# Kernel tuning notes

Hardware: AMD Instinct MI355X
Metric: run time of the kernel (lower is better)

The kernel has to match this reference:

```python
import jax, jax.numpy as jnp
import numpy as np

N_NODES = 50000
N_EDGES = 800000
N_GRAPHS = 128
IN_DIM = 256
OUT_DIM = 128
N_LAYERS = 3
NEG_SLOPE = 0.01  # nn.LeakyReLU default


def setup_inputs() -> dict:
    key = jax.random.key(0)
    ks = jax.random.split(key, 10)
    feat = jax.random.normal(ks[0], (N_NODES, IN_DIM), jnp.float32)
    src = jax.random.randint(ks[1], (N_EDGES,), 0, N_NODES, jnp.int32)
    dst = jax.random.randint(ks[2], (N_EDGES,), 0, N_NODES, jnp.int32)
    graph_ids = jnp.sort(jax.random.randint(ks[3], (N_NODES,), 0, N_GRAPHS, jnp.int32))
    s_in = 1.0 / np.sqrt(IN_DIM).astype(np.float32)
    s_out = 1.0 / np.sqrt(OUT_DIM).astype(np.float32)
    w_red = jax.random.uniform(ks[4], (IN_DIM, OUT_DIM), jnp.float32, -s_in, s_in)
    b_red = jax.random.uniform(ks[5], (OUT_DIM,), jnp.float32, -s_in, s_in)
    w_gcn = jax.random.uniform(ks[6], (N_LAYERS, OUT_DIM, OUT_DIM), jnp.float32, -s_out, s_out)
    b_gcn = jnp.zeros((N_LAYERS, OUT_DIM), jnp.float32)  # DGL GraphConv bias init = zeros
    w_cls = jax.random.uniform(ks[7], (OUT_DIM, 2), jnp.float32, -s_out, s_out)
    b_cls = jax.random.uniform(ks[8], (2,), jnp.float32, -s_out, s_out)
    return dict(feat=feat, src=src, dst=dst, graph_ids=graph_ids,
                w_red=w_red, b_red=b_red, w_gcn=w_gcn, b_gcn=b_gcn,
                w_cls=w_cls, b_cls=b_cls)


def _graph_conv(x, src, dst, w, b, out_norm, in_norm):
    # DGL GraphConv, norm='both': h = D_in^{-1/2} A D_out^{-1/2} x W + b
    xs = x * out_norm[:, None]                                   # [N, d] source normalization
    agg = jax.ops.segment_sum(xs[src], dst, num_segments=x.shape[0])  # gather -> scatter-add
    return (agg * in_norm[:, None]) @ w + b


def reference(feat, src, dst, graph_ids, w_red, b_red, w_gcn, b_gcn, w_cls, b_cls):
    n = feat.shape[0]
    ones = jnp.ones((src.shape[0],), feat.dtype)
    out_deg = jax.ops.segment_sum(ones, src, num_segments=n)
    in_deg = jax.ops.segment_sum(ones, dst, num_segments=n)
    out_norm = jnp.maximum(out_deg, 1.0) ** -0.5  # DGL clamps degree to >=1
    in_norm = jnp.maximum(in_deg, 1.0) ** -0.5
    h0 = feat @ w_red + b_red  # Dropout(0.2) in eval mode = identity
    # Faithful to source: every layer consumes h0 (node_features never updated);
    # only the last layer's activation survives the loop.
    out = h0
    for i in range(N_LAYERS):
        out = jax.nn.leaky_relu(
            _graph_conv(h0, src, dst, w_gcn[i], b_gcn[i], out_norm, in_norm), NEG_SLOPE)
    g = jax.ops.segment_sum(out, graph_ids, num_segments=N_GRAPHS)  # sum readout per graph
    return g @ w_cls + b_cls  # [N_GRAPHS, 2]
```

## Files before the change

### kernel.cpp

```cpp
#include <hip/hip_runtime.h>

#define N_NODES 50000
#define N_EDGES 800000
#define N_GRAPHS 128
#define IN_DIM 256
#define OUT_DIM 128
#define NEG_SLOPE 0.01f

#define RCHUNK 64
#define NB_SCAN ((N_NODES + 255) / 256)

#define NSLICE 4
#define SLICE 12544
#define NTOT (NSLICE * SLICE)
#define NCHUNK 64
#define NE4 (N_EDGES / 4)
#define QPC (NE4 / NCHUNK)

typedef __attribute__((ext_vector_type(8))) short bf16x8;
typedef __attribute__((ext_vector_type(4))) float f32x4;
typedef unsigned short ushort_t;
typedef unsigned int uint_t;

__device__ inline ushort_t f2b(float f) {
    union { float f; unsigned u; } c{f};
    unsigned r = c.u + 0x7FFFu + ((c.u >> 16) & 1u);
    return (ushort_t)(r >> 16);
}
__device__ inline float b2f(ushort_t u) {
    union { unsigned u; float f; } c{(unsigned)u << 16};
    return c.f;
}
__device__ inline float blo(uint_t v) {
    union { unsigned u; float f; } c{v << 16};
    return c.f;
}
__device__ inline float bhi(uint_t v) {
    union { unsigned u; float f; } c{v & 0xFFFF0000u};
    return c.f;
}

__global__ __launch_bounds__(256) void deg_kernel(const int4* __restrict__ src4,
                                                  const int4* __restrict__ dst4,
                                                  ushort_t* __restrict__ rep) {
    __shared__ uint_t bins[SLICE / 2];
    int b     = blockIdx.x;
    int hist  = b >> 8;
    int rem   = b & 255;
    int slice = rem >> 6;
    int chunk = rem & 63;
    const int4* ea = hist ? dst4 : src4;
    int lo = slice * SLICE;

    for (int i = threadIdx.x; i < SLICE / 2; i += 256) bins[i] = 0;
    __syncthreads();

    int q0 = chunk * QPC;
    int q1 = q0 + QPC;
    for (int q = q0 + threadIdx.x; q < q1; q += 256) {
        int4 e = ea[q];
        unsigned a0 = (unsigned)(e.x - lo);
        if (a0 < SLICE) atomicAdd(&bins[a0 >> 1], 1u << ((a0 & 1) << 4));
        unsigned a1 = (unsigned)(e.y - lo);
        if (a1 < SLICE) atomicAdd(&bins[a1 >> 1], 1u << ((a1 & 1) << 4));
        unsigned a2 = (unsigned)(e.z - lo);
        if (a2 < SLICE) atomicAdd(&bins[a2 >> 1], 1u << ((a2 & 1) << 4));
        unsigned a3 = (unsigned)(e.w - lo);
        if (a3 < SLICE) atomicAdd(&bins[a3 >> 1], 1u << ((a3 & 1) << 4));
    }
    __syncthreads();

    uint_t* rp32 = (uint_t*)(rep + (size_t)(hist * NCHUNK + chunk) * NTOT + lo);
    for (int i = threadIdx.x; i < SLICE / 2; i += 256)
        rp32[i] = bins[i];
}

__global__ __launch_bounds__(256) void norm_kernel(ushort_t* __restrict__ rep,
                                                   float* __restrict__ out_norm,
                                                   float* __restrict__ in_norm,
                                                   int* __restrict__ deg_in_tot,
                                                   int* __restrict__ bsum) {
    __shared__ int red[256];
    int t = threadIdx.x;
    int i = blockIdx.x * 256 + t;
    int si_keep = 0;
    if (i < N_NODES) {
        int so = 0;
#pragma unroll
        for (int c = 0; c < NCHUNK; ++c) so += rep[(size_t)c * NTOT + i];
        int si = 0;
#pragma unroll
        for (int c = 0; c < NCHUNK; ++c) {
            size_t off = (size_t)(NCHUNK + c) * NTOT + i;
            int v = rep[off];
            rep[off] = (ushort_t)si;
            si += v;
        }
        deg_in_tot[i] = si;
        si_keep = si;
        int dq = so > 1 ? so : 1;
        int di = si > 1 ? si : 1;
        out_norm[i] = rsqrtf((float)dq);
        in_norm[i]  = rsqrtf((float)di);
    }
    red[t] = si_keep;
    __syncthreads();
    for (int off = 128; off > 0; off >>= 1) {
        if (t < off) red[t] += red[t + off];
        __syncthreads();
    }
    if (t == 0) bsum[blockIdx.x] = red[0];
}

__global__ __launch_bounds__(256) void fillwc_kernel(const int* __restrict__ deg_in,
                                                     const int* __restrict__ bsum,
                                                     int* __restrict__ row_ofs,
                                                     const float* __restrict__ w_red,
                                                     const float* __restrict__ b_red,
                                                     const float* __restrict__ w2,
                                                     ushort_t* __restrict__ Wcs,
                                                     float* __restrict__ bc,
                                                     float* __restrict__ g) {
    int t   = threadIdx.x;
    int bid = blockIdx.x;

    if (bid < NB_SCAN) {
        __shared__ int sh[256];
        int v = (t < NB_SCAN) ? bsum[t] : 0;
        sh[t] = v;
        __syncthreads();
        for (int off = 1; off < 256; off <<= 1) {
            int a = sh[t];
            int b = (t >= off) ? sh[t - off] : 0;
            __syncthreads();
            sh[t] = a + b;
            __syncthreads();
        }
        int bofs  = sh[bid] - bsum[bid];
        int total = sh[NB_SCAN - 1];
        __syncthreads();

        int idx = bid * 256 + t;
        int dv  = (idx < N_NODES) ? deg_in[idx] : 0;
        sh[t] = dv;
        __syncthreads();
        for (int off = 1; off < 256; off <<= 1) {
            int a = sh[t];
            int b = (t >= off) ? sh[t - off] : 0;
            __syncthreads();
            sh[t] = a + b;
            __syncthreads();
        }
        if (idx < N_NODES) row_ofs[idx] = bofs + sh[t] - dv;
        if (bid == 0 && t == 0) row_ofs[N_NODES] = total;
    } else if (t < OUT_DIM) {
        int i = bid - NB_SCAN;
        int j = t;
        if (i < N_GRAPHS) g[i * OUT_DIM + j] = 0.f;
        const float* vin = (i < IN_DIM) ? (w_red + (size_t)i * OUT_DIM) : b_red;
        float s = 0.f;
        for (int k = 0; k < OUT_DIM; ++k) s = fmaf(vin[k], w2[k * OUT_DIM + j], s);
        if (i < IN_DIM) Wcs[(size_t)j * IN_DIM + i] = f2b(s);
        else            bc[j] = s;
    }
}

__global__ __launch_bounds__(256) void build_kernel(const int4* __restrict__ src4,
                                                    const int4* __restrict__ dst4,
                                                    const int* __restrict__ row_ofs,
                                                    const ushort_t* __restrict__ rep,
                                                    int* __restrict__ esrc) {
    __shared__ int cur[SLICE];
    int b     = blockIdx.x;
    int slice = b >> 6;
    int chunk = b & 63;
    int lo    = slice * SLICE;
    const ushort_t* rel = rep + (size_t)(NCHUNK + chunk) * NTOT + lo;

    for (int i = threadIdx.x; i < SLICE; i += 256) {
        int n = lo + i;
        int r = (n < N_NODES) ? row_ofs[n] : 0;
        cur[i] = r + (int)rel[i];
    }
    __syncthreads();

    int q0 = chunk * QPC;
    int q1 = q0 + QPC;
    for (int q = q0 + threadIdx.x; q < q1; q += 256) {
        int4 s = src4[q];
        int4 d = dst4[q];
        unsigned a0 = (unsigned)(d.x - lo); if (a0 < SLICE) esrc[atomicAdd(&cur[a0], 1)] = s.x;
        unsigned a1 = (unsigned)(d.y - lo); if (a1 < SLICE) esrc[atomicAdd(&cur[a1], 1)] = s.y;
        unsigned a2 = (unsigned)(d.z - lo); if (a2 < SLICE) esrc[atomicAdd(&cur[a2], 1)] = s.z;
        unsigned a3 = (unsigned)(d.w - lo); if (a3 < SLICE) esrc[atomicAdd(&cur[a3], 1)] = s.w;
    }
}

__global__ __launch_bounds__(256) void gemm_z(const float* __restrict__ feat,
                                              const ushort_t* __restrict__ Wcs,
                                              const float* __restrict__ bc,
                                              const float* __restrict__ out_norm,
                                              ushort_t* __restrict__ zb) {
    __shared__ ushort_t Bs[64 * IN_DIM];
    int t    = threadIdx.x;
    int lane = t & 63;
    int wv   = t >> 6;
    int bm   = blockIdx.x * 64 + wv * 16;
    int bn0  = blockIdx.y * 64;
    int mrow = lane & 15;
    int kg   = lane >> 4;
    int gm   = bm + mrow;

    {
        const char* wsrc = (const char*)(Wcs + (size_t)bn0 * IN_DIM);
        char* bdst = (char*)Bs;
#pragma unroll
        for (int p = 0; p < 8; ++p) {
            int d  = p * 4096 + t * 16;
            int ds = d ^ (((d >> 9) & 7) << 4);
            *(int4*)(bdst + ds) = *(const int4*)(wsrc + d);
        }
    }
    __syncthreads();

    f32x4 acc[4];
#pragma unroll
    for (int nt = 0; nt < 4; ++nt) acc[nt] = (f32x4){0.f, 0.f, 0.f, 0.f};

    int boff[4];
#pragma unroll
    for (int nt = 0; nt < 4; ++nt) {
        int n = nt * 16 + mrow;
        boff[nt] = n * 512 + ((kg * 16) ^ ((n & 7) << 4));
    }
    const char* bsp = (const char*)Bs;

    bool valid = gm < N_NODES;
    const float* fp = feat + (size_t)(valid ? gm : 0) * IN_DIM + kg * 8;
    const float4 zf4 = make_float4(0.f, 0.f, 0.f, 0.f);

    float4 a0c = valid ? *(const float4*)(fp + 0) : zf4;
    float4 a1c = valid ? *(const float4*)(fp + 4) : zf4;
    float4 a0n = zf4, a1n = zf4;

#pragma unroll
    for (int kt = 0; kt < IN_DIM / 32; ++kt) {
        if (kt < IN_DIM / 32 - 1) {
            a0n = valid ? *(const float4*)(fp + (kt + 1) * 32) : zf4;
            a1n = valid ? *(const float4*)(fp + (kt + 1) * 32 + 4) : zf4;
        }
        bf16x8 af;
        af[0] = (short)f2b(a0c.x); af[1] = (short)f2b(a0c.y);
        af[2] = (short)f2b(a0c.z); af[3] = (short)f2b(a0c.w);
        af[4] = (short)f2b(a1c.x); af[5] = (short)f2b(a1c.y);
        af[6] = (short)f2b(a1c.z); af[7] = (short)f2b(a1c.w);
#pragma unroll
        for (int nt = 0; nt < 4; ++nt) {
            bf16x8 bf = *(const bf16x8*)(bsp + (boff[nt] ^ (kt << 6)));
            acc[nt] = __builtin_amdgcn_mfma_f32_16x16x32_bf16(af, bf, acc[nt], 0, 0, 0);
        }
        a0c = a0n; a1c = a1n;
    }

    float on[4];
#pragma unroll
    for (int r = 0; r < 4; ++r) {
        int row = bm + kg * 4 + r;
        on[r] = (row < N_NODES) ? out_norm[row] : 0.f;
    }
#pragma unroll
    for (int nt = 0; nt < 4; ++nt) {
        int col = bn0 + nt * 16 + mrow;
        float bcv = bc[col];
#pragma unroll
        for (int r = 0; r < 4; ++r) {
            int row = bm + kg * 4 + r;
            if (row < N_NODES)
                zb[(size_t)row * OUT_DIM + col] = f2b(on[r] * (acc[nt][r] + bcv));
        }
    }
}

__global__ __launch_bounds__(256) void gather_kernel(const uint4* __restrict__ zb4,
                                                     const int* __restrict__ esrc,
                                                     const int* __restrict__ row_ofs,
                                                     const float* __restrict__ in_norm,
                                                     const float* __restrict__ b2,
                                                     uint4* __restrict__ hb4) {
    int n      = blockIdx.x * 16 + (threadIdx.x >> 4);
    int lane16 = threadIdx.x & 15;
    int e0 = row_ofs[n];
    int e1 = row_ofs[n + 1];
    float ac[8];
#pragma unroll
    for (int i = 0; i < 8; ++i) ac[i] = 0.f;

    int e = e0;
    for (; e + 8 <= e1; e += 8) {
        uint4 v[8];
#pragma unroll
        for (int u = 0; u < 8; ++u) v[u] = zb4[(size_t)esrc[e + u] * 16 + lane16];
#pragma unroll
        for (int u = 0; u < 8; ++u) {
            ac[0] += blo(v[u].x); ac[1] += bhi(v[u].x);
            ac[2] += blo(v[u].y); ac[3] += bhi(v[u].y);
            ac[4] += blo(v[u].z); ac[5] += bhi(v[u].z);
            ac[6] += blo(v[u].w); ac[7] += bhi(v[u].w);
        }
    }
    if (e + 4 <= e1) {
        uint4 v[4];
#pragma unroll
        for (int u = 0; u < 4; ++u) v[u] = zb4[(size_t)esrc[e + u] * 16 + lane16];
#pragma unroll
        for (int u = 0; u < 4; ++u) {
            ac[0] += blo(v[u].x); ac[1] += bhi(v[u].x);
            ac[2] += blo(v[u].y); ac[3] += bhi(v[u].y);
            ac[4] += blo(v[u].z); ac[5] += bhi(v[u].z);
            ac[6] += blo(v[u].w); ac[7] += bhi(v[u].w);
        }
        e += 4;
    }
    for (; e < e1; ++e) {
        uint4 v = zb4[(size_t)esrc[e] * 16 + lane16];
        ac[0] += blo(v.x); ac[1] += bhi(v.x);
        ac[2] += blo(v.y); ac[3] += bhi(v.y);
        ac[4] += blo(v.z); ac[5] += bhi(v.z);
        ac[6] += blo(v.w); ac[7] += bhi(v.w);
    }

    float inn = in_norm[n];
    float4 bA = *(const float4*)&b2[lane16 * 8];
    float4 bB = *(const float4*)&b2[lane16 * 8 + 4];
    float hv[8];
    hv[0] = fmaf(inn, ac[0], bA.x); hv[1] = fmaf(inn, ac[1], bA.y);
    hv[2] = fmaf(inn, ac[2], bA.z); hv[3] = fmaf(inn, ac[3], bA.w);
    hv[4] = fmaf(inn, ac[4], bB.x); hv[5] = fmaf(inn, ac[5], bB.y);
    hv[6] = fmaf(inn, ac[6], bB.z); hv[7] = fmaf(inn, ac[7], bB.w);
#pragma unroll
    for (int i = 0; i < 8; ++i) hv[i] = (hv[i] > 0.f) ? hv[i] : NEG_SLOPE * hv[i];
    uint4 o;
    o.x = (uint_t)f2b(hv[0]) | ((uint_t)f2b(hv[1]) << 16);
    o.y = (uint_t)f2b(hv[2]) | ((uint_t)f2b(hv[3]) << 16);
    o.z = (uint_t)f2b(hv[4]) | ((uint_t)f2b(hv[5]) << 16);
    o.w = (uint_t)f2b(hv[6]) | ((uint_t)f2b(hv[7]) << 16);
    hb4[(size_t)n * 16 + lane16] = o;
}

__global__ __launch_bounds__(64) void readout_kernel(const uint_t* __restrict__ hb2,
                                                     const int* __restrict__ gids,
                                                     float* __restrict__ g) {
    int t    = threadIdx.x;
    int n0   = blockIdx.x * RCHUNK;
    int nend = n0 + RCHUNK;
    if (nend > N_NODES) nend = N_NODES;
    float acc0 = 0.f, acc1 = 0.f;
    int   cur = gids[n0];
    for (int n = n0; n < nend; ++n) {
        int gid = gids[n];
        if (gid != cur) {
            atomicAdd(&g[cur * OUT_DIM + 2 * t], acc0);
            atomicAdd(&g[cur * OUT_DIM + 2 * t + 1], acc1);
            acc0 = acc1 = 0.f;
            cur = gid;
        }
        uint_t v = hb2[(size_t)n * 64 + t];
        acc0 += blo(v);
        acc1 += bhi(v);
    }
    atomicAdd(&g[cur * OUT_DIM + 2 * t], acc0);
    atomicAdd(&g[cur * OUT_DIM + 2 * t + 1], acc1);
}

__global__ __launch_bounds__(256) void cls_kernel(const float* __restrict__ g,
                                                  const float* __restrict__ w_cls,
                                                  const float* __restrict__ b_cls,
                                                  float* __restrict__ out) {
    int t  = threadIdx.x;
    int gr = t >> 1;
    int c  = t & 1;
    float s = b_cls[c];
    for (int k = 0; k < OUT_DIM; ++k) s = fmaf(g[gr * OUT_DIM + k], w_cls[k * 2 + c], s);
    out[t] = s;
}

extern "C" void kernel_launch(void* const* d_in, const int* in_sizes, int n_in,
                              void* d_out, int out_size, void* d_ws, size_t ws_size,
                              hipStream_t stream) {
    const float* feat  = (const float*)d_in[0];
    const int*   src   = (const int*)d_in[1];
    const int*   dst   = (const int*)d_in[2];
    const int*   gids  = (const int*)d_in[3];
    const float* w_red = (const float*)d_in[4];
    const float* b_red = (const float*)d_in[5];
    const float* w_gcn = (const float*)d_in[6];
    const float* b_gcn = (const float*)d_in[7];
    const float* w_cls = (const float*)d_in[8];
    const float* b_cls = (const float*)d_in[9];
    float* out = (float*)d_out;

    float* z        = (float*)d_ws;
    float* h        = z + (size_t)N_NODES * OUT_DIM;
    float* out_norm = h + (size_t)N_NODES * OUT_DIM;
    float* in_norm  = out_norm + N_NODES;
    int*   deg_in   = (int*)(in_norm + N_NODES);
    int*   row_ofs  = deg_in + N_NODES;
    int*   esrc     = row_ofs + N_NODES + 1;
    int*   bsum     = esrc + N_EDGES;
    ushort_t* Wcs   = (ushort_t*)(bsum + NB_SCAN);
    float* bc       = (float*)(Wcs + IN_DIM * OUT_DIM);
    float* g        = bc + OUT_DIM;

    ushort_t* zb = (ushort_t*)z;
    ushort_t* hb = (ushort_t*)h;

    ushort_t* rep = (ushort_t*)z;

    const float* w2 = w_gcn + 2 * OUT_DIM * OUT_DIM;
    const float* b2 = b_gcn + 2 * OUT_DIM;

    deg_kernel<<<2 * NSLICE * NCHUNK, 256, 0, stream>>>((const int4*)src, (const int4*)dst, rep);
    norm_kernel<<<NB_SCAN, 256, 0, stream>>>(rep, out_norm, in_norm, deg_in, bsum);
    fillwc_kernel<<<NB_SCAN + IN_DIM + 1, 256, 0, stream>>>(deg_in, bsum, row_ofs,
                                                            w_red, b_red, w2, Wcs, bc, g);
    build_kernel<<<NSLICE * NCHUNK, 256, 0, stream>>>((const int4*)src, (const int4*)dst,
                                                      row_ofs, rep, esrc);
    gemm_z<<<dim3((N_NODES + 63) / 64, 2), 256, 0, stream>>>(feat, Wcs, bc, out_norm, zb);
    gather_kernel<<<N_NODES / 16, 256, 0, stream>>>((const uint4*)zb, esrc, row_ofs,
                                                    in_norm, b2, (uint4*)hb);
    readout_kernel<<<(N_NODES + RCHUNK - 1) / RCHUNK, 64, 0, stream>>>((const uint_t*)hb,
                                                                       gids, g);
    cls_kernel<<<1, 256, 0, stream>>>(g, w_cls, b_cls, out);
}
```

Measured before the change: 151.2 us.

## Fuse readout and classifier into gather; store edge sources as 16-bit

```diff
diff --git a/kernel.cpp b/kernel.cpp
--- a/kernel.cpp
+++ b/kernel.cpp
@@ -7,7 +7,6 @@
 #define OUT_DIM 128
 #define NEG_SLOPE 0.01f
 
-#define RCHUNK 64
 #define NB_SCAN ((N_NODES + 255) / 256)
 
 #define NSLICE 4
@@ -26,10 +25,6 @@
     union { float f; unsigned u; } c{f};
     unsigned r = c.u + 0x7FFFu + ((c.u >> 16) & 1u);
     return (ushort_t)(r >> 16);
-}
-__device__ inline float b2f(ushort_t u) {
-    union { unsigned u; float f; } c{(unsigned)u << 16};
-    return c.f;
 }
 __device__ inline float blo(uint_t v) {
     union { unsigned u; float f; } c{v << 16};
@@ -120,7 +115,8 @@
                                                      const float* __restrict__ w2,
                                                      ushort_t* __restrict__ Wcs,
                                                      float* __restrict__ bc,
-                                                     float* __restrict__ g) {
+                                                     const float* __restrict__ b_cls,
+                                                     float* __restrict__ out) {
     int t   = threadIdx.x;
     int bid = blockIdx.x;
 
@@ -153,15 +149,17 @@
         }
         if (idx < N_NODES) row_ofs[idx] = bofs + sh[t] - dv;
         if (bid == 0 && t == 0) row_ofs[N_NODES] = total;
-    } else if (t < OUT_DIM) {
-        int i = bid - NB_SCAN;
-        int j = t;
-        if (i < N_GRAPHS) g[i * OUT_DIM + j] = 0.f;
-        const float* vin = (i < IN_DIM) ? (w_red + (size_t)i * OUT_DIM) : b_red;
-        float s = 0.f;
-        for (int k = 0; k < OUT_DIM; ++k) s = fmaf(vin[k], w2[k * OUT_DIM + j], s);
-        if (i < IN_DIM) Wcs[(size_t)j * IN_DIM + i] = f2b(s);
-        else            bc[j] = s;
+    } else {
+        if (bid == NB_SCAN) out[t] = b_cls[t & 1];
+        if (t < OUT_DIM) {
+            int i = bid - NB_SCAN;
+            int j = t;
+            const float* vin = (i < IN_DIM) ? (w_red + (size_t)i * OUT_DIM) : b_red;
+            float s = 0.f;
+            for (int k = 0; k < OUT_DIM; ++k) s = fmaf(vin[k], w2[k * OUT_DIM + j], s);
+            if (i < IN_DIM) Wcs[(size_t)j * IN_DIM + i] = f2b(s);
+            else            bc[j] = s;
+        }
     }
 }
 
@@ -169,7 +167,7 @@
                                                     const int4* __restrict__ dst4,
                                                     const int* __restrict__ row_ofs,
                                                     const ushort_t* __restrict__ rep,
-                                                    int* __restrict__ esrc) {
+                                                    ushort_t* __restrict__ esrc) {
     __shared__ int cur[SLICE];
     int b     = blockIdx.x;
     int slice = b >> 6;
@@ -189,10 +187,10 @@
     for (int q = q0 + threadIdx.x; q < q1; q += 256) {
         int4 s = src4[q];
         int4 d = dst4[q];
-        unsigned a0 = (unsigned)(d.x - lo); if (a0 < SLICE) esrc[atomicAdd(&cur[a0], 1)] = s.x;
-        unsigned a1 = (unsigned)(d.y - lo); if (a1 < SLICE) esrc[atomicAdd(&cur[a1], 1)] = s.y;
-        unsigned a2 = (unsigned)(d.z - lo); if (a2 < SLICE) esrc[atomicAdd(&cur[a2], 1)] = s.z;
-        unsigned a3 = (unsigned)(d.w - lo); if (a3 < SLICE) esrc[atomicAdd(&cur[a3], 1)] = s.w;
+        unsigned a0 = (unsigned)(d.x - lo); if (a0 < SLICE) esrc[atomicAdd(&cur[a0], 1)] = (ushort_t)s.x;
+        unsigned a1 = (unsigned)(d.y - lo); if (a1 < SLICE) esrc[atomicAdd(&cur[a1], 1)] = (ushort_t)s.y;
+        unsigned a2 = (unsigned)(d.z - lo); if (a2 < SLICE) esrc[atomicAdd(&cur[a2], 1)] = (ushort_t)s.z;
+        unsigned a3 = (unsigned)(d.w - lo); if (a3 < SLICE) esrc[atomicAdd(&cur[a3], 1)] = (ushort_t)s.w;
     }
 }
 
@@ -282,11 +280,16 @@
 }
 
 __global__ __launch_bounds__(256) void gather_kernel(const uint4* __restrict__ zb4,
-                                                     const int* __restrict__ esrc,
+                                                     const ushort_t* __restrict__ esrc,
                                                      const int* __restrict__ row_ofs,
                                                      const float* __restrict__ in_norm,
                                                      const float* __restrict__ b2,
-                                                     uint4* __restrict__ hb4) {
+                                                     const int* __restrict__ gids,
+                                                     const float* __restrict__ w_cls,
+                                                     float* __restrict__ out) {
+    __shared__ int   pg[16];
+    __shared__ float pp0[16], pp1[16];
+
     int n      = blockIdx.x * 16 + (threadIdx.x >> 4);
     int lane16 = threadIdx.x & 15;
     int e0 = row_ofs[n];
@@ -339,49 +342,42 @@
     hv[6] = fmaf(inn, ac[6], bB.z); hv[7] = fmaf(inn, ac[7], bB.w);
 #pragma unroll
     for (int i = 0; i < 8; ++i) hv[i] = (hv[i] > 0.f) ? hv[i] : NEG_SLOPE * hv[i];
-    uint4 o;
-    o.x = (uint_t)f2b(hv[0]) | ((uint_t)f2b(hv[1]) << 16);
-    o.y = (uint_t)f2b(hv[2]) | ((uint_t)f2b(hv[3]) << 16);
-    o.z = (uint_t)f2b(hv[4]) | ((uint_t)f2b(hv[5]) << 16);
-    o.w = (uint_t)f2b(hv[6]) | ((uint_t)f2b(hv[7]) << 16);
-    hb4[(size_t)n * 16 + lane16] = o;
-}
-
-__global__ __launch_bounds__(64) void readout_kernel(const uint_t* __restrict__ hb2,
-                                                     const int* __restrict__ gids,
-                                                     float* __restrict__ g) {
-    int t    = threadIdx.x;
-    int n0   = blockIdx.x * RCHUNK;
-    int nend = n0 + RCHUNK;
-    if (nend > N_NODES) nend = N_NODES;
-    float acc0 = 0.f, acc1 = 0.f;
-    int   cur = gids[n0];
-    for (int n = n0; n < nend; ++n) {
-        int gid = gids[n];
-        if (gid != cur) {
-            atomicAdd(&g[cur * OUT_DIM + 2 * t], acc0);
-            atomicAdd(&g[cur * OUT_DIM + 2 * t + 1], acc1);
-            acc0 = acc1 = 0.f;
-            cur = gid;
-        }
-        uint_t v = hb2[(size_t)n * 64 + t];
-        acc0 += blo(v);
-        acc1 += bhi(v);
-    }
-    atomicAdd(&g[cur * OUT_DIM + 2 * t], acc0);
-    atomicAdd(&g[cur * OUT_DIM + 2 * t + 1], acc1);
-}
-
-__global__ __launch_bounds__(256) void cls_kernel(const float* __restrict__ g,
-                                                  const float* __restrict__ w_cls,
-                                                  const float* __restrict__ b_cls,
-                                                  float* __restrict__ out) {
-    int t  = threadIdx.x;
-    int gr = t >> 1;
-    int c  = t & 1;
-    float s = b_cls[c];
-    for (int k = 0; k < OUT_DIM; ++k) s = fmaf(g[gr * OUT_DIM + k], w_cls[k * 2 + c], s);
-    out[t] = s;
+
+    float p0 = 0.f, p1 = 0.f;
+#pragma unroll
+    for (int k = 0; k < 4; ++k) {
+        float4 q = ((const float4*)w_cls)[lane16 * 4 + k];
+        p0 += hv[2 * k] * q.x + hv[2 * k + 1] * q.z;
+        p1 += hv[2 * k] * q.y + hv[2 * k + 1] * q.w;
+    }
+#pragma unroll
+    for (int off = 8; off > 0; off >>= 1) {
+        p0 += __shfl_down(p0, off, 16);
+        p1 += __shfl_down(p1, off, 16);
+    }
+    if (lane16 == 0) {
+        int qw = threadIdx.x >> 4;
+        pg[qw]  = gids[n];
+        pp0[qw] = p0;
+        pp1[qw] = p1;
+    }
+    __syncthreads();
+    if (threadIdx.x == 0) {
+        int cg = pg[0];
+        float a0 = 0.f, a1 = 0.f;
+        for (int j = 0; j < 16; ++j) {
+            if (pg[j] != cg) {
+                atomicAdd(&out[cg * 2 + 0], a0);
+                atomicAdd(&out[cg * 2 + 1], a1);
+                cg = pg[j];
+                a0 = a1 = 0.f;
+            }
+            a0 += pp0[j];
+            a1 += pp1[j];
+        }
+        atomicAdd(&out[cg * 2 + 0], a0);
+        atomicAdd(&out[cg * 2 + 1], a1);
+    }
 }
 
 extern "C" void kernel_launch(void* const* d_in, const int* in_sizes, int n_in,
@@ -400,19 +396,16 @@
     float* out = (float*)d_out;
 
     float* z        = (float*)d_ws;
-    float* h        = z + (size_t)N_NODES * OUT_DIM;
-    float* out_norm = h + (size_t)N_NODES * OUT_DIM;
+    float* out_norm = z + (size_t)N_NODES * OUT_DIM;
     float* in_norm  = out_norm + N_NODES;
     int*   deg_in   = (int*)(in_norm + N_NODES);
     int*   row_ofs  = deg_in + N_NODES;
-    int*   esrc     = row_ofs + N_NODES + 1;
-    int*   bsum     = esrc + N_EDGES;
+    ushort_t* esrc  = (ushort_t*)(row_ofs + N_NODES + 1);
+    int*   bsum     = (int*)(esrc + N_EDGES);
     ushort_t* Wcs   = (ushort_t*)(bsum + NB_SCAN);
     float* bc       = (float*)(Wcs + IN_DIM * OUT_DIM);
-    float* g        = bc + OUT_DIM;
 
     ushort_t* zb = (ushort_t*)z;
-    ushort_t* hb = (ushort_t*)h;
 
     ushort_t* rep = (ushort_t*)z;
 
@@ -422,13 +415,11 @@
     deg_kernel<<<2 * NSLICE * NCHUNK, 256, 0, stream>>>((const int4*)src, (const int4*)dst, rep);
     norm_kernel<<<NB_SCAN, 256, 0, stream>>>(rep, out_norm, in_norm, deg_in, bsum);
     fillwc_kernel<<<NB_SCAN + IN_DIM + 1, 256, 0, stream>>>(deg_in, bsum, row_ofs,
-                                                            w_red, b_red, w2, Wcs, bc, g);
+                                                            w_red, b_red, w2, Wcs, bc,
+                                                            b_cls, out);
     build_kernel<<<NSLICE * NCHUNK, 256, 0, stream>>>((const int4*)src, (const int4*)dst,
                                                       row_ofs, rep, esrc);
     gemm_z<<<dim3((N_NODES + 63) / 64, 2), 256, 0, stream>>>(feat, Wcs, bc, out_norm, zb);
     gather_kernel<<<N_NODES / 16, 256, 0, stream>>>((const uint4*)zb, esrc, row_ofs,
-                                                    in_norm, b2, (uint4*)hb);
-    readout_kernel<<<(N_NODES + RCHUNK - 1) / RCHUNK, 64, 0, stream>>>((const uint_t*)hb,
-                                                                       gids, g);
-    cls_kernel<<<1, 256, 0, stream>>>(g, w_cls, b_cls, out);
-}
+                                                    in_norm, b2, gids, w_cls, out);
+}
```

Result: faster. 140.9 us (-6.8%).
